# Kernel tuning notes

Measured on AMD Instinct MI355X. Metric: run time of the kernel, lower is better.

Reference implementation:

```python
import jax, jax.numpy as jnp
import numpy as np

B, D, K, L, H = 16384, 1024, 512, 128, 64  # batch, input_dim, num_components, latent_dim, phi hidden
EPS = 1e-9


def setup_inputs() -> dict:
    key = jax.random.key(0)
    k0, k1, k2, k3 = jax.random.split(key, 4)
    # small scales keep squared distances O(1-10) so exp(-d2) is non-degenerate
    x = jax.random.normal(k0, (B, D), jnp.float32) * 0.03
    z_samples = jax.random.normal(k1, (K, L), jnp.float32)
    W1 = jax.random.normal(k2, (L, H), jnp.float32) * (1.0 / np.sqrt(L)).astype(np.float32)
    b1 = jnp.zeros((H,), jnp.float32)
    W2 = jax.random.normal(k3, (H, D), jnp.float32) * 0.01
    b2 = jnp.zeros((D,), jnp.float32)
    return {"x": x, "z_samples": z_samples, "W1": W1, "b1": b1, "W2": W2, "b2": b2}


def reference(x, z_samples, W1, b1, W2, b2):
    # PhiNet: Linear -> ReLU -> Linear, applied to all components at once
    phi = jnp.maximum(z_samples @ W1 + b1, 0.0) @ W2 + b2          # (K, D)
    # ||x - phi_k||^2 for all (k, b) via GEMM expansion (fuses the per-component loop)
    sq = (jnp.sum(phi * phi, axis=-1)[:, None]
          + jnp.sum(x * x, axis=-1)[None, :]
          - 2.0 * (phi @ x.T))                                      # (K, B)
    lik = jnp.exp(-sq)                                              # (K, B)
    # weights = 1/K; sum_k w * lik = mean over K
    mixture_ll = jnp.log(jnp.mean(lik, axis=0) + EPS)               # (B,)
    return mixture_ll.mean()
```

## Files before the change

kernel.cpp:

```cpp
#include <hip/hip_runtime.h>
#include <hip/hip_bf16.h>
#include <stdint.h>

#define N_B   16384
#define D_DIM 1024
#define K_K   512
#define L_DIM 128
#define H_DIM 64
#define SX    1032

typedef __attribute__((ext_vector_type(8))) short short8;
typedef __attribute__((ext_vector_type(4))) float f32x4;

__device__ __forceinline__ unsigned short f2bf(float f) {
    union { float f; unsigned int u; } c; c.f = f;
    unsigned int u = c.u;
    unsigned int r = (u + 0x7FFFu + ((u >> 16) & 1u)) >> 16;
    return (unsigned short)r;
}

__device__ __forceinline__ unsigned int pk2(float a, float b) {
    __hip_bfloat162 t = __float22bfloat162_rn(make_float2(a, b));
    union { __hip_bfloat162 h; unsigned int u; } c; c.h = t;
    return c.u;
}

__global__ __launch_bounds__(256) void prep_kernel(
    const float* __restrict__ z, const float* __restrict__ W1,
    const float* __restrict__ b1, const float* __restrict__ W2,
    const float* __restrict__ b2, unsigned short* __restrict__ W2bf,
    unsigned short* __restrict__ h_bf, float* __restrict__ phi2) {
    __shared__ float zsh[8][L_DIM];
    __shared__ float hsh[8][H_DIM];
    __shared__ float redp[4][8];
    const int tid = threadIdx.x;
    const int k0 = blockIdx.x * 8;

    {
        int i = blockIdx.x * 256 + tid;
        float4 v = ((const float4*)W2)[i];
        uint2 o = make_uint2(pk2(v.x, v.y), pk2(v.z, v.w));
        *(uint2*)(W2bf + i * 4) = o;
    }
#pragma unroll
    for (int c = 0; c < 4; ++c) {
        int idx = c * 256 + tid;
        zsh[idx >> 7][idx & 127] = z[k0 * L_DIM + idx];
    }
    __syncthreads();
    {
        const int j = tid & 63, kk = tid >> 6;
        float bb = b1[j];
        float s0 = bb, s1 = bb;
        for (int l = 0; l < L_DIM; ++l) {
            float w = W1[l * H_DIM + j];
            s0 += zsh[kk][l] * w;
            s1 += zsh[kk + 4][l] * w;
        }
        float h0 = fmaxf(s0, 0.0f), h1 = fmaxf(s1, 0.0f);
        hsh[kk][j] = h0; hsh[kk + 4][j] = h1;
        h_bf[(k0 + kk) * H_DIM + j]     = f2bf(h0);
        h_bf[(k0 + kk + 4) * H_DIM + j] = f2bf(h1);
    }
    __syncthreads();
    float ss[8] = {0.f, 0.f, 0.f, 0.f, 0.f, 0.f, 0.f, 0.f};
#pragma unroll
    for (int c = 0; c < 4; ++c) {
        int d = c * 256 + tid;
        float bb = b2[d];
        float a[8];
#pragma unroll
        for (int kk = 0; kk < 8; ++kk) a[kk] = bb;
        for (int j = 0; j < H_DIM; ++j) {
            float w = W2[j * D_DIM + d];
#pragma unroll
            for (int kk = 0; kk < 8; ++kk) a[kk] += hsh[kk][j] * w;
        }
#pragma unroll
        for (int kk = 0; kk < 8; ++kk) ss[kk] += a[kk] * a[kk];
    }
    const int lane = tid & 63, wv = tid >> 6;
#pragma unroll
    for (int kk = 0; kk < 8; ++kk) {
        float v = ss[kk];
#pragma unroll
        for (int o = 1; o < 64; o <<= 1) v += __shfl_xor(v, o, 64);
        if (lane == 0) redp[wv][kk] = v;
    }
    __syncthreads();
    if (tid < 8) phi2[k0 + tid] = redp[0][tid] + redp[1][tid] + redp[2][tid] + redp[3][tid];
}

__global__ __launch_bounds__(256) void main_kernel(
    const float* __restrict__ x, const unsigned short* __restrict__ W2bf,
    const unsigned short* __restrict__ h_bf, const float* __restrict__ phi2,
    const float* __restrict__ b2, float* __restrict__ out) {
    __shared__ __align__(16) unsigned short x_bf[32 * SX];
    __shared__ __align__(16) unsigned short u_tile[32 * 72];
    __shared__ float phi2s[K_K];
    __shared__ float x2s[32], xb2s[32];
    __shared__ float red[4][32];

    const int tid = threadIdx.x;
    const int wv  = tid >> 6;
    const int l   = tid & 63;
    const int lm  = l & 15;
    const int q   = l >> 4;
    const int n0  = blockIdx.x * 32;

    float4 b2r[4];
#pragma unroll
    for (int sub = 0; sub < 4; ++sub)
        b2r[sub] = ((const float4*)b2)[sub * 64 + l];

    phi2s[tid]       = phi2[tid];
    phi2s[256 + tid] = phi2[256 + tid];

    float x2a[8], xba[8];
#pragma unroll
    for (int batch = 0; batch < 2; ++batch) {
        const int r0 = wv * 8 + batch * 4;
        float4 xv[16];
#pragma unroll
        for (int s = 0; s < 4; ++s)
#pragma unroll
            for (int sub = 0; sub < 4; ++sub)
                xv[s * 4 + sub] = *(const float4*)(x + (size_t)(n0 + r0 + s) * D_DIM + sub * 256 + l * 4);
#pragma unroll
        for (int s = 0; s < 4; ++s) {
            float s2 = 0.f, sb = 0.f;
#pragma unroll
            for (int sub = 0; sub < 4; ++sub) {
                float4 v = xv[s * 4 + sub];
                s2 += v.x*v.x + v.y*v.y + v.z*v.z + v.w*v.w;
                sb += v.x*b2r[sub].x + v.y*b2r[sub].y + v.z*b2r[sub].z + v.w*b2r[sub].w;
                uint2 o = make_uint2(pk2(v.x, v.y), pk2(v.z, v.w));
                *(uint2*)&x_bf[(r0 + s) * SX + sub * 256 + l * 4] = o;
            }
            x2a[batch * 4 + s] = s2; xba[batch * 4 + s] = sb;
        }
    }
#pragma unroll
    for (int s = 0; s < 8; ++s) {
        float a = x2a[s], b = xba[s];
#pragma unroll
        for (int o = 1; o < 64; o <<= 1) { a += __shfl_xor(a, o, 64); b += __shfl_xor(b, o, 64); }
        if (l == 0) { x2s[wv * 8 + s] = a; xb2s[wv * 8 + s] = b; }
    }
    __syncthreads();

    const unsigned short* w2row = W2bf + (size_t)(wv * 16 + lm) * D_DIM + q * 8;
    short8 wf[8];
#pragma unroll
    for (int p = 0; p < 8; ++p)
        wf[p] = *(const short8*)(w2row + p * 32);
    f32x4 c1[2] = {};
#pragma unroll
    for (int ks = 0; ks < 32; ++ks) {
        const int k0 = ks * 32 + q * 8;
        short8 bw = wf[ks & 7];
        if (ks < 24)
            wf[ks & 7] = *(const short8*)(w2row + (ks + 8) * 32);
        short8 a0 = *(const short8*)&x_bf[lm * SX + k0];
        short8 a1 = *(const short8*)&x_bf[(16 + lm) * SX + k0];
        c1[0] = __builtin_amdgcn_mfma_f32_16x16x32_bf16(a0, bw, c1[0], 0, 0, 0);
        c1[1] = __builtin_amdgcn_mfma_f32_16x16x32_bf16(a1, bw, c1[1], 0, 0, 0);
    }
#pragma unroll
    for (int i = 0; i < 2; ++i)
#pragma unroll
        for (int r = 0; r < 4; ++r)
            u_tile[(i * 16 + q * 4 + r) * 72 + wv * 16 + lm] = f2bf(c1[i][r]);
    __syncthreads();

    f32x4 acc[8][2] = {};
#pragma unroll
    for (int ks = 0; ks < 2; ++ks) {
        const int ko = ks * 32 + q * 8;
        short8 bfr[2];
#pragma unroll
        for (int j = 0; j < 2; ++j)
            bfr[j] = *(const short8*)&u_tile[(j * 16 + lm) * 72 + ko];
#pragma unroll
        for (int i = 0; i < 8; ++i) {
            short8 a = *(const short8*)(h_bf + (size_t)(wv * 128 + i * 16 + lm) * H_DIM + ko);
#pragma unroll
            for (int j = 0; j < 2; ++j)
                acc[i][j] = __builtin_amdgcn_mfma_f32_16x16x32_bf16(a, bfr[j], acc[i][j], 0, 0, 0);
        }
    }
    float xn0 = x2s[lm]      - 2.f * xb2s[lm];
    float xn1 = x2s[16 + lm] - 2.f * xb2s[16 + lm];
    float cs0 = 0.f, cs1 = 0.f;
#pragma unroll
    for (int i = 0; i < 8; ++i) {
#pragma unroll
        for (int r = 0; r < 4; ++r) {
            float p2 = phi2s[wv * 128 + i * 16 + q * 4 + r];
            cs0 += __expf(-(p2 + xn0 - 2.f * acc[i][0][r]));
            cs1 += __expf(-(p2 + xn1 - 2.f * acc[i][1][r]));
        }
    }
    cs0 += __shfl_xor(cs0, 16, 64); cs0 += __shfl_xor(cs0, 32, 64);
    cs1 += __shfl_xor(cs1, 16, 64); cs1 += __shfl_xor(cs1, 32, 64);
    if (l < 16) { red[wv][l] = cs0; red[wv][16 + l] = cs1; }
    __syncthreads();
    if (tid < 32) {
        float row_lik = red[0][tid] + red[1][tid] + red[2][tid] + red[3][tid];
        float lg = __logf(row_lik * (1.0f / (float)K_K) + 1e-9f);
        lg += __shfl_xor(lg, 1, 64);
        lg += __shfl_xor(lg, 2, 64);
        lg += __shfl_xor(lg, 4, 64);
        lg += __shfl_xor(lg, 8, 64);
        lg += __shfl_xor(lg, 16, 64);
        if (tid == 0) atomicAdd(out, lg * (1.0f / (float)N_B));
    }
}

extern "C" void kernel_launch(void* const* d_in, const int* in_sizes, int n_in,
                              void* d_out, int out_size, void* d_ws, size_t ws_size,
                              hipStream_t stream) {
    const float* x  = (const float*)d_in[0];
    const float* z  = (const float*)d_in[1];
    const float* W1 = (const float*)d_in[2];
    const float* b1 = (const float*)d_in[3];
    const float* W2 = (const float*)d_in[4];
    const float* b2 = (const float*)d_in[5];

    char* ws = (char*)d_ws;
    unsigned short* W2bf = (unsigned short*)(ws);
    unsigned short* h_bf = (unsigned short*)(ws + 131072);
    float*          phi2 = (float*)(ws + 196608);

    hipMemsetAsync(d_out, 0, sizeof(float), stream);
    prep_kernel<<<64, 256, 0, stream>>>(z, W1, b1, W2, b2, W2bf, h_bf, phi2);
    main_kernel<<<N_B / 32, 256, 0, stream>>>(x, W2bf, h_bf, phi2, b2, (float*)d_out);
}
```

Measured before the change: 145.9 us.

## Spread prep kernel over more blocks and batch all x loads up front

```diff
diff --git a/kernel.cpp b/kernel.cpp
--- a/kernel.cpp
+++ b/kernel.cpp
@@ -30,68 +30,62 @@
     const float* __restrict__ b1, const float* __restrict__ W2,
     const float* __restrict__ b2, unsigned short* __restrict__ W2bf,
     unsigned short* __restrict__ h_bf, float* __restrict__ phi2) {
-    __shared__ float zsh[8][L_DIM];
-    __shared__ float hsh[8][H_DIM];
-    __shared__ float redp[4][8];
+    __shared__ float zsh[2][L_DIM];
+    __shared__ float hsh[2][H_DIM];
+    __shared__ float redp[4][2];
     const int tid = threadIdx.x;
-    const int k0 = blockIdx.x * 8;
-
-    {
-        int i = blockIdx.x * 256 + tid;
+    const int k0 = blockIdx.x * 2;
+
+    if (tid < 64) {
+        int i = blockIdx.x * 64 + tid;
         float4 v = ((const float4*)W2)[i];
         uint2 o = make_uint2(pk2(v.x, v.y), pk2(v.z, v.w));
         *(uint2*)(W2bf + i * 4) = o;
     }
+    zsh[tid >> 7][tid & 127] = z[k0 * L_DIM + tid];
+    __syncthreads();
+    if (tid < 128) {
+        const int j = tid & 63, kk = tid >> 6;
+        float s = b1[j];
+#pragma unroll 8
+        for (int l = 0; l < L_DIM; ++l)
+            s += zsh[kk][l] * W1[l * H_DIM + j];
+        float h = fmaxf(s, 0.0f);
+        hsh[kk][j] = h;
+        h_bf[(k0 + kk) * H_DIM + j] = f2bf(h);
+    }
+    __syncthreads();
+    float a0[4], a1[4];
 #pragma unroll
     for (int c = 0; c < 4; ++c) {
-        int idx = c * 256 + tid;
-        zsh[idx >> 7][idx & 127] = z[k0 * L_DIM + idx];
-    }
-    __syncthreads();
-    {
-        const int j = tid & 63, kk = tid >> 6;
-        float bb = b1[j];
-        float s0 = bb, s1 = bb;
-        for (int l = 0; l < L_DIM; ++l) {
-            float w = W1[l * H_DIM + j];
-            s0 += zsh[kk][l] * w;
-            s1 += zsh[kk + 4][l] * w;
-        }
-        float h0 = fmaxf(s0, 0.0f), h1 = fmaxf(s1, 0.0f);
-        hsh[kk][j] = h0; hsh[kk + 4][j] = h1;
-        h_bf[(k0 + kk) * H_DIM + j]     = f2bf(h0);
-        h_bf[(k0 + kk + 4) * H_DIM + j] = f2bf(h1);
-    }
-    __syncthreads();
-    float ss[8] = {0.f, 0.f, 0.f, 0.f, 0.f, 0.f, 0.f, 0.f};
-#pragma unroll
-    for (int c = 0; c < 4; ++c) {
-        int d = c * 256 + tid;
-        float bb = b2[d];
-        float a[8];
-#pragma unroll
-        for (int kk = 0; kk < 8; ++kk) a[kk] = bb;
-        for (int j = 0; j < H_DIM; ++j) {
-            float w = W2[j * D_DIM + d];
-#pragma unroll
-            for (int kk = 0; kk < 8; ++kk) a[kk] += hsh[kk][j] * w;
-        }
-#pragma unroll
-        for (int kk = 0; kk < 8; ++kk) ss[kk] += a[kk] * a[kk];
-    }
+        float bb = b2[c * 256 + tid];
+        a0[c] = bb; a1[c] = bb;
+    }
+#pragma unroll 8
+    for (int j = 0; j < H_DIM; ++j) {
+        float h0 = hsh[0][j], h1 = hsh[1][j];
+#pragma unroll
+        for (int c = 0; c < 4; ++c) {
+            float w = W2[j * D_DIM + c * 256 + tid];
+            a0[c] += h0 * w;
+            a1[c] += h1 * w;
+        }
+    }
+    float ss0 = 0.f, ss1 = 0.f;
+#pragma unroll
+    for (int c = 0; c < 4; ++c) { ss0 += a0[c] * a0[c]; ss1 += a1[c] * a1[c]; }
     const int lane = tid & 63, wv = tid >> 6;
 #pragma unroll
-    for (int kk = 0; kk < 8; ++kk) {
-        float v = ss[kk];
-#pragma unroll
-        for (int o = 1; o < 64; o <<= 1) v += __shfl_xor(v, o, 64);
-        if (lane == 0) redp[wv][kk] = v;
-    }
-    __syncthreads();
-    if (tid < 8) phi2[k0 + tid] = redp[0][tid] + redp[1][tid] + redp[2][tid] + redp[3][tid];
-}
-
-__global__ __launch_bounds__(256) void main_kernel(
+    for (int o = 1; o < 64; o <<= 1) {
+        ss0 += __shfl_xor(ss0, o, 64);
+        ss1 += __shfl_xor(ss1, o, 64);
+    }
+    if (lane == 0) { redp[wv][0] = ss0; redp[wv][1] = ss1; }
+    __syncthreads();
+    if (tid < 2) phi2[k0 + tid] = redp[0][tid] + redp[1][tid] + redp[2][tid] + redp[3][tid];
+}
+
+__global__ __launch_bounds__(256, 2) void main_kernel(
     const float* __restrict__ x, const unsigned short* __restrict__ W2bf,
     const unsigned short* __restrict__ h_bf, const float* __restrict__ phi2,
     const float* __restrict__ b2, float* __restrict__ out) {
@@ -116,29 +110,27 @@
     phi2s[tid]       = phi2[tid];
     phi2s[256 + tid] = phi2[256 + tid];
 
+    float4 xv[32];
+    const float* xbase = x + (size_t)(n0 + wv * 8) * D_DIM + l * 4;
+#pragma unroll
+    for (int s = 0; s < 8; ++s)
+#pragma unroll
+        for (int sub = 0; sub < 4; ++sub)
+            xv[s * 4 + sub] = *(const float4*)(xbase + (size_t)s * D_DIM + sub * 256);
+
     float x2a[8], xba[8];
 #pragma unroll
-    for (int batch = 0; batch < 2; ++batch) {
-        const int r0 = wv * 8 + batch * 4;
-        float4 xv[16];
-#pragma unroll
-        for (int s = 0; s < 4; ++s)
-#pragma unroll
-            for (int sub = 0; sub < 4; ++sub)
-                xv[s * 4 + sub] = *(const float4*)(x + (size_t)(n0 + r0 + s) * D_DIM + sub * 256 + l * 4);
-#pragma unroll
-        for (int s = 0; s < 4; ++s) {
-            float s2 = 0.f, sb = 0.f;
-#pragma unroll
-            for (int sub = 0; sub < 4; ++sub) {
-                float4 v = xv[s * 4 + sub];
-                s2 += v.x*v.x + v.y*v.y + v.z*v.z + v.w*v.w;
-                sb += v.x*b2r[sub].x + v.y*b2r[sub].y + v.z*b2r[sub].z + v.w*b2r[sub].w;
-                uint2 o = make_uint2(pk2(v.x, v.y), pk2(v.z, v.w));
-                *(uint2*)&x_bf[(r0 + s) * SX + sub * 256 + l * 4] = o;
-            }
-            x2a[batch * 4 + s] = s2; xba[batch * 4 + s] = sb;
-        }
+    for (int s = 0; s < 8; ++s) {
+        float s2 = 0.f, sb = 0.f;
+#pragma unroll
+        for (int sub = 0; sub < 4; ++sub) {
+            float4 v = xv[s * 4 + sub];
+            s2 += v.x*v.x + v.y*v.y + v.z*v.z + v.w*v.w;
+            sb += v.x*b2r[sub].x + v.y*b2r[sub].y + v.z*b2r[sub].z + v.w*b2r[sub].w;
+            uint2 o = make_uint2(pk2(v.x, v.y), pk2(v.z, v.w));
+            *(uint2*)&x_bf[(wv * 8 + s) * SX + sub * 256 + l * 4] = o;
+        }
+        x2a[s] = s2; xba[s] = sb;
     }
 #pragma unroll
     for (int s = 0; s < 8; ++s) {
@@ -233,6 +225,6 @@
     float*          phi2 = (float*)(ws + 196608);
 
     hipMemsetAsync(d_out, 0, sizeof(float), stream);
-    prep_kernel<<<64, 256, 0, stream>>>(z, W1, b1, W2, b2, W2bf, h_bf, phi2);
+    prep_kernel<<<256, 256, 0, stream>>>(z, W1, b1, W2, b2, W2bf, h_bf, phi2);
     main_kernel<<<N_B / 32, 256, 0, stream>>>(x, W2bf, h_bf, phi2, b2, (float*)d_out);
 }
```

New measurement: 125.8 us. 13.7% less time.
